# Kernel optimization log

Hardware: AMD Instinct MI355X
Metric: run time of the kernel (lower is better)

## Reference

```python
import jax, jax.numpy as jnp
import numpy as np

N_DRUGS = 4096
W_DIM = 512
N_SUB = 10
N_EDGES = 131072


def setup_inputs() -> dict:
    key = jax.random.key(0)
    k1, k2, k3, k4 = jax.random.split(key, 4)
    z_drug = jax.random.normal(k1, (N_DRUGS, W_DIM), dtype=jnp.float32)
    # glorot-ish init for weights
    global_weight = jax.random.normal(k2, (W_DIM, W_DIM), dtype=jnp.float32) * (2.0 / (2 * W_DIM)) ** 0.5
    local_diag = jax.random.normal(k3, (N_SUB, W_DIM), dtype=jnp.float32) * (2.0 / (W_DIM + 1)) ** 0.5
    batch_edges = jax.random.randint(k4, (2, N_EDGES), 0, N_DRUGS, dtype=jnp.int64)
    return {
        "z_drug": z_drug,
        "global_weight": global_weight,
        "local_diag": local_diag,
        "batch_edges": batch_edges,
        "edge_sub_type_idx": 2,
    }


def reference(z_drug, global_weight, local_diag, batch_edges, edge_sub_type_idx):
    # edge_type == 'drug_drug': z1 = z2 = z_drug
    row_embed = z_drug[batch_edges[0]]            # [B, D]
    col_embed = z_drug[batch_edges[1]]            # [B, D]
    d = local_diag[edge_sub_type_idx]             # [D] diagonal of local weight matrix
    # row @ diag(d) @ W @ diag(d) == ((row * d) @ W) * d
    p = ((row_embed * d) @ global_weight) * d     # [B, D]
    # diagonal(p @ col^T) == rowwise dot product
    score = jnp.sum(p * col_embed, axis=-1)       # [B]
    return jax.nn.sigmoid(score)
```

## Files before the change

kernel.cpp:

```cpp
#include <hip/hip_runtime.h>
#include <cstdint>

#define ND 4096
#define D  512

typedef __bf16 bf16x8 __attribute__((ext_vector_type(8)));
typedef float floatx4 __attribute__((ext_vector_type(4)));
typedef unsigned short ushort8 __attribute__((ext_vector_type(8)));

__device__ __forceinline__ float bf2f(unsigned short b) {
    return __uint_as_float(((unsigned int)b) << 16);
}
__device__ __forceinline__ unsigned short f2bf(float f) {
    unsigned int u = __float_as_uint(f);
    u += 0x7fffu + ((u >> 16) & 1u);
    return (unsigned short)(u >> 16);
}
__device__ __forceinline__ float lo16(unsigned int u) { return __uint_as_float(u << 16); }
__device__ __forceinline__ float hi16(unsigned int u) { return __uint_as_float(u & 0xffff0000u); }

__device__ __forceinline__ void gll16(const void* g, void* l) {
    __builtin_amdgcn_global_load_lds((const __attribute__((address_space(1))) unsigned int*)g,
                                     (__attribute__((address_space(3))) unsigned int*)l,
                                     16, 0, 0);
}

union U8B8 { ushort8 u; bf16x8 b; };

__device__ __forceinline__ int2 detect_flags(const unsigned short* z, const int* ed) {
    int lane = threadIdx.x & 63;
    unsigned short u = z[lane];
    int e = (u >> 7) & 0xFF;
    unsigned long long b0 = __ballot(e >= 96 && e <= 160);
    unsigned long long b1 = __ballot(ed[2 * lane + 1] == 0);
    int2 f;
    f.x = (__popcll(b0) >= 56) ? 1 : 0;
    f.y = (__popcll(b1) >= 56) ? 1 : 0;
    return f;
}

__global__ __launch_bounds__(256) void make_mt(const void* __restrict__ Wv,
                                               const void* __restrict__ ldv,
                                               const int* __restrict__ sub,
                                               unsigned short* __restrict__ Mt,
                                               const unsigned short* __restrict__ zdet,
                                               const int* __restrict__ eddet) {
    __shared__ float xp[64][65];
    int2 f = detect_flags(zdet, eddet);
    int bf = f.x;
    int su = sub[0];
    if ((unsigned)su > 9u) su = 2;
    int k0 = (blockIdx.x & 7) * 64, n0 = (blockIdx.x >> 3) * 64;
    int j = threadIdx.x & 63, w = threadIdx.x >> 6;
#pragma unroll
    for (int r = 0; r < 16; r++) {
        int k = k0 + w * 16 + r;
        float v = bf ? bf2f(((const unsigned short*)Wv)[k * D + n0 + j])
                     : ((const float*)Wv)[k * D + n0 + j];
        xp[w * 16 + r][j] = v;
    }
    __syncthreads();
    int k = k0 + j;
    float dk = bf ? bf2f(((const unsigned short*)ldv)[su * D + k])
                  : ((const float*)ldv)[su * D + k];
#pragma unroll
    for (int r = 0; r < 16; r++) {
        int n = n0 + w * 16 + r;
        float dn = bf ? bf2f(((const unsigned short*)ldv)[su * D + n])
                      : ((const float*)ldv)[su * D + n];
        Mt[n * D + k] = f2bf(xp[j][w * 16 + r] * dk * dn);
    }
}

template <bool BF>
__device__ void gemm_body(const void* __restrict__ z, const unsigned short* __restrict__ Mt,
                          unsigned short* __restrict__ Y) {
    __shared__ __bf16 As[8 * 512];
    __shared__ __bf16 Bs[8 * 512];
    int tid = threadIdx.x;
    int w = tid >> 6, lane = tid & 63;
    int rl = lane & 15, quad = lane >> 4;
    int tm = (blockIdx.x >> 3) * 64, tn = (blockIdx.x & 7) * 64;
    int wm = (w >> 1) * 32, wn = (w & 1) * 32;

    floatx4 acc[2][2] = {};
    for (int kk = 0; kk < D; kk += 64) {
        __syncthreads();
#pragma unroll
        for (int t = 0; t < 2; t++) {
            int kb = w * 2 + t;
            gll16(Mt + (tn + lane) * D + kk + kb * 8, Bs + kb * 512);
            if constexpr (BF) {
                gll16((const __bf16*)z + (tm + lane) * D + kk + kb * 8, As + kb * 512);
            } else {
                const float* zf = (const float*)z + (tm + lane) * D + kk + kb * 8;
                float4 f0 = *(const float4*)zf;
                float4 f1 = *(const float4*)(zf + 4);
                U8B8 cv;
                cv.u[0] = f2bf(f0.x); cv.u[1] = f2bf(f0.y); cv.u[2] = f2bf(f0.z); cv.u[3] = f2bf(f0.w);
                cv.u[4] = f2bf(f1.x); cv.u[5] = f2bf(f1.y); cv.u[6] = f2bf(f1.z); cv.u[7] = f2bf(f1.w);
                *(bf16x8*)(As + kb * 512 + lane * 8) = cv.b;
            }
        }
        __syncthreads();
#pragma unroll
        for (int kc = 0; kc < 64; kc += 32) {
            int kb0 = kc >> 3;
            bf16x8 a0 = *(const bf16x8*)(As + (kb0 + quad) * 512 + (wm + rl) * 8);
            bf16x8 a1 = *(const bf16x8*)(As + (kb0 + quad) * 512 + (wm + 16 + rl) * 8);
            bf16x8 b0 = *(const bf16x8*)(Bs + (kb0 + quad) * 512 + (wn + rl) * 8);
            bf16x8 b1 = *(const bf16x8*)(Bs + (kb0 + quad) * 512 + (wn + 16 + rl) * 8);
            acc[0][0] = __builtin_amdgcn_mfma_f32_16x16x32_bf16(a0, b0, acc[0][0], 0, 0, 0);
            acc[0][1] = __builtin_amdgcn_mfma_f32_16x16x32_bf16(a0, b1, acc[0][1], 0, 0, 0);
            acc[1][0] = __builtin_amdgcn_mfma_f32_16x16x32_bf16(a1, b0, acc[1][0], 0, 0, 0);
            acc[1][1] = __builtin_amdgcn_mfma_f32_16x16x32_bf16(a1, b1, acc[1][1], 0, 0, 0);
        }
    }
#pragma unroll
    for (int j = 0; j < 2; j++) {
        int col = tn + wn + j * 16 + rl;
#pragma unroll
        for (int i = 0; i < 2; i++) {
            int rbase = tm + wm + i * 16 + quad * 4;
#pragma unroll
            for (int r = 0; r < 4; r++)
                Y[(rbase + r) * D + col] = f2bf(acc[i][j][r]);
        }
    }
}

__global__ __launch_bounds__(256) void gemm_kernel(const void* __restrict__ z,
                                                   const unsigned short* __restrict__ Mt,
                                                   unsigned short* __restrict__ Y,
                                                   const int* __restrict__ eddet) {
    int2 f = detect_flags((const unsigned short*)z, eddet);
    if (f.x) gemm_body<true>(z, Mt, Y);
    else     gemm_body<false>(z, Mt, Y);
}

template <bool BF, bool I64>
__device__ void edge_slice_body(const unsigned short* __restrict__ Y,
                                const void* __restrict__ z,
                                const int* __restrict__ ed,
                                float* __restrict__ partial, int E) {
    int slice = blockIdx.x & 7;
    int egrp  = blockIdx.x >> 3;
    int lane = threadIdx.x & 63;
    int w = threadIdx.x >> 6;
    int e = egrp * 32 + w * 8 + (lane >> 3);
    int l = lane & 7;
    if (e >= E) return;
    int r, c;
    if constexpr (I64) { r = ed[2 * e]; c = ed[2 * (E + e)]; }
    else               { r = ed[e];     c = ed[E + e]; }
    r &= ND - 1; c &= ND - 1;

    int col = slice * 64 + l * 8;
    uint4 yu = *(const uint4*)(Y + r * D + col);
    float s;
    if constexpr (BF) {
        uint4 zu = *(const uint4*)((const unsigned short*)z + c * D + col);
        s  = lo16(yu.x) * lo16(zu.x) + hi16(yu.x) * hi16(zu.x);
        s += lo16(yu.y) * lo16(zu.y) + hi16(yu.y) * hi16(zu.y);
        s += lo16(yu.z) * lo16(zu.z) + hi16(yu.z) * hi16(zu.z);
        s += lo16(yu.w) * lo16(zu.w) + hi16(yu.w) * hi16(zu.w);
    } else {
        const float* zf = (const float*)z + c * D + col;
        float4 f0 = *(const float4*)zf;
        float4 f1 = *(const float4*)(zf + 4);
        s  = lo16(yu.x) * f0.x + hi16(yu.x) * f0.y;
        s += lo16(yu.y) * f0.z + hi16(yu.y) * f0.w;
        s += lo16(yu.z) * f1.x + hi16(yu.z) * f1.y;
        s += lo16(yu.w) * f1.z + hi16(yu.w) * f1.w;
    }
    s += __shfl_xor(s, 1, 64);
    s += __shfl_xor(s, 2, 64);
    s += __shfl_xor(s, 4, 64);
    if (l == 0)
        atomicAdd(partial + e, s);
}

__global__ __launch_bounds__(256) void edge_slice(const unsigned short* __restrict__ Y,
                                                  const void* __restrict__ z,
                                                  const int* __restrict__ ed,
                                                  float* __restrict__ partial, int E) {
    int2 f = detect_flags((const unsigned short*)z, ed);
    if (f.x) { if (f.y) edge_slice_body<true, true >(Y, z, ed, partial, E);
               else     edge_slice_body<true, false>(Y, z, ed, partial, E); }
    else     { if (f.y) edge_slice_body<false, true >(Y, z, ed, partial, E);
               else     edge_slice_body<false, false>(Y, z, ed, partial, E); }
}

__global__ __launch_bounds__(256) void finish_kernel(const float* __restrict__ partial,
                                                     const unsigned short* __restrict__ zdet,
                                                     const int* __restrict__ eddet,
                                                     void* __restrict__ out, int E) {
    int2 f = detect_flags(zdet, eddet);
    int e = blockIdx.x * 256 + threadIdx.x;
    if (e >= E) return;
    float t = partial[e];
    if (!(t > -1e30f && t < 1e30f)) t = 0.0f;
    float sig = 1.0f / (1.0f + __expf(-t));
    if (f.x) ((unsigned short*)out)[e] = f2bf(sig);
    else     ((float*)out)[e] = sig;
}

extern "C" void kernel_launch(void* const* d_in, const int* in_sizes, int n_in,
                              void* d_out, int out_size, void* d_ws, size_t ws_size,
                              hipStream_t stream) {
    const void* z     = d_in[0];
    const void* W     = d_in[1];
    const void* ldiag = d_in[2];
    const int* edges  = (const int*)d_in[3];
    const int* sub    = (const int*)d_in[4];
    int E = out_size;

    char* ws = (char*)d_ws;
    unsigned short* Y  = (unsigned short*)ws;
    unsigned short* Mt = (unsigned short*)(ws + 4194304);
    float* partial     = (float*)(ws + 4194304 + 524288);

    make_mt<<<64, 256, 0, stream>>>(W, ldiag, sub, Mt, (const unsigned short*)z, edges);
    gemm_kernel<<<512, 256, 0, stream>>>(z, Mt, Y, edges);
    hipMemsetAsync(partial, 0, (size_t)E * 4, stream);
    int sblocks = ((E + 31) / 32) * 8;
    edge_slice<<<sblocks, 256, 0, stream>>>(Y, z, edges, partial, E);
    finish_kernel<<<(E + 255) / 256, 256, 0, stream>>>(partial, (const unsigned short*)z,
                                                       edges, d_out, E);
}
```

Baseline: 121.6 us.

## Replace atomic edge reduction with per-slice partial buffers and thread-per-edge

The edge kernel now assigns one thread per edge per 64-column slice, looping over the slice instead of splitting it across 8 lanes with shuffles. It writes per-slice partial sums to a slice-major buffer instead of using atomicAdd, which removes the memset. The finish kernel sums the 8 partials. The GEMM block-to-tile mapping is also reordered to iterate M fastest. This trades atomics and shuffles for less coalesced per-lane row accesses and a larger partial buffer.

```diff
diff --git a/kernel.cpp b/kernel.cpp
--- a/kernel.cpp
+++ b/kernel.cpp
@@ -80,7 +80,7 @@
     int tid = threadIdx.x;
     int w = tid >> 6, lane = tid & 63;
     int rl = lane & 15, quad = lane >> 4;
-    int tm = (blockIdx.x >> 3) * 64, tn = (blockIdx.x & 7) * 64;
+    int tm = (blockIdx.x & 63) * 64, tn = (blockIdx.x >> 6) * 64;
     int wm = (w >> 1) * 32, wn = (w & 1) * 32;
 
     floatx4 acc[2][2] = {};
@@ -144,40 +144,39 @@
                                 const int* __restrict__ ed,
                                 float* __restrict__ partial, int E) {
     int slice = blockIdx.x & 7;
-    int egrp  = blockIdx.x >> 3;
-    int lane = threadIdx.x & 63;
-    int w = threadIdx.x >> 6;
-    int e = egrp * 32 + w * 8 + (lane >> 3);
-    int l = lane & 7;
+    int e = (blockIdx.x >> 3) * 256 + threadIdx.x;
     if (e >= E) return;
     int r, c;
     if constexpr (I64) { r = ed[2 * e]; c = ed[2 * (E + e)]; }
     else               { r = ed[e];     c = ed[E + e]; }
     r &= ND - 1; c &= ND - 1;
 
-    int col = slice * 64 + l * 8;
-    uint4 yu = *(const uint4*)(Y + r * D + col);
-    float s;
+    int col = slice * 64;
+    const uint4* yp = (const uint4*)(Y + r * D + col);
+    float s = 0.f;
     if constexpr (BF) {
-        uint4 zu = *(const uint4*)((const unsigned short*)z + c * D + col);
-        s  = lo16(yu.x) * lo16(zu.x) + hi16(yu.x) * hi16(zu.x);
-        s += lo16(yu.y) * lo16(zu.y) + hi16(yu.y) * hi16(zu.y);
-        s += lo16(yu.z) * lo16(zu.z) + hi16(yu.z) * hi16(zu.z);
-        s += lo16(yu.w) * lo16(zu.w) + hi16(yu.w) * hi16(zu.w);
+        const uint4* zp = (const uint4*)((const unsigned short*)z + c * D + col);
+#pragma unroll
+        for (int i = 0; i < 8; i++) {
+            uint4 yu = yp[i], zu = zp[i];
+            s += lo16(yu.x) * lo16(zu.x) + hi16(yu.x) * hi16(zu.x);
+            s += lo16(yu.y) * lo16(zu.y) + hi16(yu.y) * hi16(zu.y);
+            s += lo16(yu.z) * lo16(zu.z) + hi16(yu.z) * hi16(zu.z);
+            s += lo16(yu.w) * lo16(zu.w) + hi16(yu.w) * hi16(zu.w);
+        }
     } else {
-        const float* zf = (const float*)z + c * D + col;
-        float4 f0 = *(const float4*)zf;
-        float4 f1 = *(const float4*)(zf + 4);
-        s  = lo16(yu.x) * f0.x + hi16(yu.x) * f0.y;
-        s += lo16(yu.y) * f0.z + hi16(yu.y) * f0.w;
-        s += lo16(yu.z) * f1.x + hi16(yu.z) * f1.y;
-        s += lo16(yu.w) * f1.z + hi16(yu.w) * f1.w;
-    }
-    s += __shfl_xor(s, 1, 64);
-    s += __shfl_xor(s, 2, 64);
-    s += __shfl_xor(s, 4, 64);
-    if (l == 0)
-        atomicAdd(partial + e, s);
+        const float4* zp = (const float4*)((const float*)z + c * D + col);
+#pragma unroll
+        for (int i = 0; i < 8; i++) {
+            uint4 yu = yp[i];
+            float4 f0 = zp[2 * i], f1 = zp[2 * i + 1];
+            s += lo16(yu.x) * f0.x + hi16(yu.x) * f0.y;
+            s += lo16(yu.y) * f0.z + hi16(yu.y) * f0.w;
+            s += lo16(yu.z) * f1.x + hi16(yu.z) * f1.y;
+            s += lo16(yu.w) * f1.z + hi16(yu.w) * f1.w;
+        }
+    }
+    partial[slice * E + e] = s;
 }
 
 __global__ __launch_bounds__(256) void edge_slice(const unsigned short* __restrict__ Y,
@@ -198,7 +197,10 @@
     int2 f = detect_flags(zdet, eddet);
     int e = blockIdx.x * 256 + threadIdx.x;
     if (e >= E) return;
-    float t = partial[e];
+    float t = 0.f;
+#pragma unroll
+    for (int s = 0; s < 8; s++)
+        t += partial[s * E + e];
     if (!(t > -1e30f && t < 1e30f)) t = 0.0f;
     float sig = 1.0f / (1.0f + __expf(-t));
     if (f.x) ((unsigned short*)out)[e] = f2bf(sig);
@@ -222,8 +224,7 @@
 
     make_mt<<<64, 256, 0, stream>>>(W, ldiag, sub, Mt, (const unsigned short*)z, edges);
     gemm_kernel<<<512, 256, 0, stream>>>(z, Mt, Y, edges);
-    hipMemsetAsync(partial, 0, (size_t)E * 4, stream);
-    int sblocks = ((E + 31) / 32) * 8;
+    int sblocks = ((E + 255) / 256) * 8;
     edge_slice<<<sblocks, 256, 0, stream>>>(Y, z, edges, partial, E);
     finish_kernel<<<(E + 255) / 256, 256, 0, stream>>>(partial, (const unsigned short*)z,
                                                        edges, d_out, E);
```

Result: slower. 139.9 us (+15.0%).
